# Performance work log

Measured on AMD Instinct MI355X. Metric: run time of the kernel, lower is better.

The kernel has to match this reference:

```python
import jax, jax.numpy as jnp
import numpy as np
from jax import lax

EPS = 1e-6

def rms_norm(x, w):
    return x * lax.rsqrt(jnp.mean(x * x, axis=-1, keepdims=True) + EPS) * w

def rec_layer(x, conv_w, conv_b, Wr_w, Wr_b, Wi_w, Wi_b, log_a, out_w, norm_w):
    # x: [B, L, d]; depthwise causal conv, kernel size 4
    B, L, d = x.shape
    xc = lax.conv_general_dilated(
        x.transpose(0, 2, 1), conv_w, window_strides=(1,), padding=[(3, 0)],
        dimension_numbers=("NCH", "OIH", "NCH"), feature_group_count=d)
    x_conv = xc.transpose(0, 2, 1) + conv_b  # [B, L, d]
    r_t = jax.nn.sigmoid(x_conv @ Wr_w.T + Wr_b)
    i_t = jax.nn.sigmoid(x_conv @ Wi_w.T + Wi_b)
    a_base = jax.nn.sigmoid(log_a)  # [d]
    a_t = jnp.power(a_base, 8.0 * r_t)  # [B, L, d]
    u_t = i_t * x_conv

    def step(h, au):
        a, u = au
        h = a * h + jnp.sqrt(jnp.clip(1.0 - a * a, 0.0, None)) * u
        return h, h

    _, hs = lax.scan(step, jnp.zeros((B, d), x.dtype),
                     (a_t.transpose(1, 0, 2), u_t.transpose(1, 0, 2)))
    out = hs.transpose(1, 0, 2)  # [B, L, d]
    return rms_norm(out @ out_w.T, norm_w)

def setup_inputs() -> dict:
    B, L, M, d, do = 8, 2048, 256, 1024, 256
    key = jax.random.key(0)
    ks = jax.random.split(key, 24)
    inp = {
        "concept_out": jax.random.normal(ks[0], (B, M, d), jnp.float32),
        "encoder_out": jax.random.normal(ks[1], (B, L, d), jnp.float32),
        "boundary_probs": jax.random.uniform(ks[2], (B, L), jnp.float32),
        "boundary_idx": jnp.sort(jax.random.randint(ks[3], (B, M), 0, L, jnp.int32), axis=1),
        "gate_w": jax.random.normal(ks[4], (d, d), jnp.float32) * 0.02,
        "gate_b": jnp.zeros((d,), jnp.float32),
        "down_w": jax.random.normal(ks[5], (do, d), jnp.float32) * 0.02,
        "up_w": jax.random.normal(ks[6], (d, do), jnp.float32) * 0.02,
        "norm_out_w": jnp.ones((d,), jnp.float32),
        "rec_conv_w": jax.random.normal(ks[7], (3, do, 1, 4), jnp.float32) * 0.02,
        "rec_conv_b": jnp.zeros((3, do), jnp.float32),
        "rec_Wr_w": jax.random.normal(ks[8], (3, do, do), jnp.float32) * 0.02,
        "rec_Wr_b": jnp.zeros((3, do), jnp.float32),
        "rec_Wi_w": jax.random.normal(ks[9], (3, do, do), jnp.float32) * 0.02,
        "rec_Wi_b": jnp.zeros((3, do), jnp.float32),
        "rec_log_a": jnp.full((3, do), 7.5, jnp.float32),
        "rec_out_w": jax.random.normal(ks[10], (3, do, do), jnp.float32) * 0.02,
        "rec_norm_w": jnp.ones((3, do), jnp.float32),
    }
    return inp

def reference(concept_out, encoder_out, boundary_probs, boundary_idx,
              gate_w, gate_b, down_w, up_w, norm_out_w,
              rec_conv_w, rec_conv_b, rec_Wr_w, rec_Wr_b,
              rec_Wi_w, rec_Wi_b, rec_log_a, rec_out_w, rec_norm_w):
    B, L, d = encoder_out.shape
    M = concept_out.shape[1]
    # 1. EMA smoothing over boundaries
    p_at_bounds = jnp.take_along_axis(boundary_probs, boundary_idx, axis=1)  # [B, M]

    def ema_step(h, pc):
        p_i, c_i = pc  # [B], [B, d]
        h = p_i[:, None] * c_i + (1.0 - p_i[:, None]) * h
        return h, h

    _, sm = lax.scan(ema_step, jnp.zeros((B, d), concept_out.dtype),
                     (p_at_bounds.T, concept_out.transpose(1, 0, 2)))
    smoothed = sm.transpose(1, 0, 2)  # [B, M, d]
    # 2. Plug-back via searchsorted (== torch.bucketize right=True)
    arange_L = jnp.arange(L)
    counts = jax.vmap(lambda bi: jnp.searchsorted(bi, arange_L, side="right"))(boundary_idx)
    bucket = jnp.clip(counts - 1, 0, None)  # [B, L]
    plugback = jnp.take_along_axis(smoothed, bucket[..., None], axis=1)  # [B, L, d]
    # 3. Gated residual
    gate = jax.nn.sigmoid(encoder_out @ gate_w.T + gate_b)
    h = (1.0 - boundary_probs[..., None]) * gate * encoder_out + plugback
    # 4. Decoder recurrence
    h = h @ down_w.T
    for k in range(3):
        h = rec_layer(h, rec_conv_w[k], rec_conv_b[k], rec_Wr_w[k], rec_Wr_b[k],
                      rec_Wi_w[k], rec_Wi_b[k], rec_log_a[k], rec_out_w[k], rec_norm_w[k])
    h = h @ up_w.T
    return rms_norm(h, norm_out_w)
```

## Files before the change

kernel.cpp:

```cpp
#include <hip/hip_runtime.h>
#include <hip/hip_bf16.h>
#include <stdint.h>

typedef __attribute__((ext_vector_type(8))) short short8;
typedef __attribute__((ext_vector_type(4))) float f32x4;
typedef __hip_bfloat16 bf16;

#define NB   8
#define LSEQ 2048
#define NM   256
#define DMODEL 1024
#define DO   256
#define BLR  16384
#define NCH  64
#define CLK  32

__device__ __forceinline__ float sigm(float x) { return 1.f / (1.f + __expf(-x)); }

__device__ __forceinline__ void gl_lds16(const void* g, void* l) {
  __builtin_amdgcn_global_load_lds((const __attribute__((address_space(1))) void*)g,
                                   (__attribute__((address_space(3))) void*)l, 16, 0, 0);
}

__device__ __forceinline__ short8 ds_read128(const bf16* p) {
  short8 r;
  unsigned a = (unsigned)(uintptr_t)(const __attribute__((address_space(3))) bf16*)p;
  asm volatile("ds_read_b128 %0, %1" : "=v"(r) : "v"(a));
  return r;
}

__device__ __forceinline__ unsigned short bf16bits(float v) {
  bf16 b = __float2bfloat16(v);
  return *(unsigned short*)&b;
}
__device__ __forceinline__ float bits2f(unsigned short u) {
  bf16 b = *(bf16*)&u;
  return __bfloat162float(b);
}


__global__ __launch_bounds__(256) void prep_kernel(
    const float* __restrict__ encoder_out, ushort4* __restrict__ encb4,
    const float* __restrict__ gate_w, const float* __restrict__ down_w,
    const float* __restrict__ up_w, const float* __restrict__ wr_w,
    const float* __restrict__ wi_w, const float* __restrict__ ow_w,
    const float* __restrict__ log_a,
    bf16* __restrict__ gate_wb, bf16* __restrict__ down_wb, bf16* __restrict__ up_wb,
    bf16* __restrict__ wrb, bf16* __restrict__ wib, bf16* __restrict__ owb,
    float* __restrict__ e8) {
  int i = blockIdx.x * 256 + threadIdx.x;
  if (i < 4194304) {
    float4 v = ((const float4*)encoder_out)[i];
    ushort4 o;
    o.x = bf16bits(v.x); o.y = bf16bits(v.y); o.z = bf16bits(v.z); o.w = bf16bits(v.w);
    encb4[i] = o;
    return;
  }
  i -= 4194304;
  if (i < 1048576) { gate_wb[i] = __float2bfloat16(gate_w[i]); return; }
  i -= 1048576;
  if (i < 262144) { down_wb[i] = __float2bfloat16(down_w[i]); return; }
  i -= 262144;
  if (i < 262144) { up_wb[i] = __float2bfloat16(up_w[i]); return; }
  i -= 262144;
  if (i < 196608) { wrb[i] = __float2bfloat16(wr_w[i]); return; }
  i -= 196608;
  if (i < 196608) { wib[i] = __float2bfloat16(wi_w[i]); return; }
  i -= 196608;
  if (i < 196608) { owb[i] = __float2bfloat16(ow_w[i]); return; }
  i -= 196608;
  if (i < 768) {
    float ab = 1.f / (1.f + expf(-log_a[i]));
    e8[i] = 8.f * log2f(ab);
  }
}


__global__ __launch_bounds__(256) void ema_bucket_kernel(const float* __restrict__ cpt,
                                                         const float* __restrict__ bprobs,
                                                         const int* __restrict__ bidx,
                                                         float* __restrict__ smoothed,
                                                         int* __restrict__ bucket) {
  if (blockIdx.x < NB * 4) {
    int b = blockIdx.x >> 2;
    int c = ((blockIdx.x & 3) << 8) + threadIdx.x;
    __shared__ float p[NM];
    p[threadIdx.x] = bprobs[b * LSEQ + bidx[b * NM + threadIdx.x]];
    __syncthreads();
    const float* cp = cpt + (size_t)b * NM * DMODEL + c;
    float* sp = smoothed + (size_t)b * NM * DMODEL + c;
    float h = 0.f;
    for (int m = 0; m < NM; ++m) {
      float pm = p[m];
      h = pm * cp[(size_t)m * DMODEL] + (1.f - pm) * h;
      sp[(size_t)m * DMODEL] = h;
    }
  } else {
    int i = (blockIdx.x - NB * 4) * 256 + threadIdx.x;
    int b = i >> 11, l = i & 2047;
    const int* bi = bidx + b * NM;
    int lo = 0, hi = NM;
    while (lo < hi) {
      int mid = (lo + hi) >> 1;
      if (bi[mid] <= l) lo = mid + 1; else hi = mid;
    }
    int v = lo - 1;
    bucket[i] = v < 0 ? 0 : v;
  }
}


__global__ __launch_bounds__(256) void gate_plug_kernel(bf16* __restrict__ h0,
                                                        const bf16* __restrict__ encb,
                                                        const float* __restrict__ gbias,
                                                        const float* __restrict__ bprobs,
                                                        const int* __restrict__ bucket,
                                                        const float* __restrict__ smoothed) {
  const int m = blockIdx.x;
  const int t = threadIdx.x;
  const int b = m >> 11;
  const float pm1 = 1.f - bprobs[m];
  const float* srow = smoothed + ((size_t)(b * NM + bucket[m])) * DMODEL + t * 4;
  const size_t base = (size_t)m * DMODEL + t * 4;
  ushort4 gr = *(const ushort4*)(h0 + base);
  ushort4 er = *(const ushort4*)(encb + base);
  float4 sm4 = *(const float4*)srow;
  float4 gb4 = *(const float4*)(gbias + t * 4);
  ushort4 o;
  o.x = bf16bits(pm1 * sigm(bits2f(gr.x) + gb4.x) * bits2f(er.x) + sm4.x);
  o.y = bf16bits(pm1 * sigm(bits2f(gr.y) + gb4.y) * bits2f(er.y) + sm4.y);
  o.z = bf16bits(pm1 * sigm(bits2f(gr.z) + gb4.z) * bits2f(er.z) + sm4.z);
  o.w = bf16bits(pm1 * sigm(bits2f(gr.w) + gb4.w) * bits2f(er.w) + sm4.w);
  *(ushort4*)(h0 + base) = o;
}


__global__ __launch_bounds__(256) void conv_kernel(const bf16* __restrict__ x,
                                                   const float* __restrict__ cw,
                                                   const float* __restrict__ cb,
                                                   bf16* __restrict__ xcb) {
  int i4 = blockIdx.x * 256 + threadIdx.x;
  int cg = i4 & 63;
  int bl = i4 >> 6;
  int l = bl & 2047;
  int c0 = cg << 2;
  float wf[4][4];
#pragma unroll
  for (int cc = 0; cc < 4; ++cc) {
    float4 w4 = ((const float4*)cw)[c0 + cc];
    wf[cc][0] = w4.x; wf[cc][1] = w4.y; wf[cc][2] = w4.z; wf[cc][3] = w4.w;
  }
  float4 cb4 = *(const float4*)(cb + c0);
  float s0 = cb4.x, s1 = cb4.y, s2 = cb4.z, s3 = cb4.w;
#pragma unroll
  for (int kk = 0; kk < 4; ++kk) {
    int ll = l - 3 + kk;
    if (ll >= 0) {
      ushort4 xv = *(const ushort4*)(x + (size_t)(bl + kk - 3) * DO + c0);
      s0 += wf[0][kk] * bits2f(xv.x);
      s1 += wf[1][kk] * bits2f(xv.y);
      s2 += wf[2][kk] * bits2f(xv.z);
      s3 += wf[3][kk] * bits2f(xv.w);
    }
  }
  ushort4 o;
  o.x = bf16bits(s0); o.y = bf16bits(s1); o.z = bf16bits(s2); o.w = bf16bits(s3);
  *(ushort4*)(xcb + (size_t)bl * DO + c0) = o;
}


__global__ __launch_bounds__(256) void scan_p1(const unsigned int* __restrict__ ds,
                                               float2* __restrict__ AS) {
  int b = blockIdx.x / NCH, ch = blockIdx.x % NCH, c = threadIdx.x;
  size_t base = ((size_t)b * LSEQ + ch * CLK) * DO + c;
  float A = 1.f, S = 0.f;
  for (int t = 0; t < CLK; ++t) {
    unsigned int u = ds[base + (size_t)t * DO];
    float d = bits2f((unsigned short)(u & 0xffff));
    float s = bits2f((unsigned short)(u >> 16));
    float a = 1.f - d;
    A *= a;
    S = __builtin_fmaf(a, S, s);
  }
  AS[blockIdx.x * DO + c] = make_float2(A, S);
}

__global__ __launch_bounds__(256) void scan_p2(const unsigned int* __restrict__ ds,
                                               const float2* __restrict__ AS,
                                               bf16* __restrict__ hs) {
  int b = blockIdx.x / NCH, ch = blockIdx.x % NCH, c = threadIdx.x;
  float h = 0.f;
  for (int j = 0; j < ch; ++j) {
    float2 as = AS[(b * NCH + j) * DO + c];
    h = __builtin_fmaf(as.x, h, as.y);
  }
  size_t base = ((size_t)b * LSEQ + ch * CLK) * DO + c;
  for (int t = 0; t < CLK; ++t) {
    unsigned int u = ds[base + (size_t)t * DO];
    float d = bits2f((unsigned short)(u & 0xffff));
    float s = bits2f((unsigned short)(u >> 16));
    h = __builtin_fmaf(-d, h, h) + s;
    hs[base + (size_t)t * DO] = __float2bfloat16(h);
  }
}


__global__ __launch_bounds__(256) void rmsnorm1024_kernel(const bf16* __restrict__ in,
                                                          const float* __restrict__ w,
                                                          float* __restrict__ out) {
  int row = blockIdx.x, t = threadIdx.x;
  ushort4 raw = ((const ushort4*)(in + (size_t)row * 1024))[t];
  float v0 = bits2f(raw.x), v1 = bits2f(raw.y), v2 = bits2f(raw.z), v3 = bits2f(raw.w);
  float ss = v0 * v0 + v1 * v1 + v2 * v2 + v3 * v3;
#pragma unroll
  for (int ofs = 32; ofs > 0; ofs >>= 1) ss += __shfl_down(ss, ofs, 64);
  __shared__ float wsum[4];
  if ((t & 63) == 0) wsum[t >> 6] = ss;
  __syncthreads();
  float tot = wsum[0] + wsum[1] + wsum[2] + wsum[3];
  float sc = rsqrtf(tot * (1.f / 1024.f) + 1e-6f);
  float4 wv = ((const float4*)w)[t];
  float4 o;
  o.x = v0 * sc * wv.x; o.y = v1 * sc * wv.y;
  o.z = v2 * sc * wv.z; o.w = v3 * sc * wv.w;
  ((float4*)(out + (size_t)row * 1024))[t] = o;
}


template <int NC, int KC>
__global__ __launch_bounds__(256, 4) void gemm_t64(const bf16* __restrict__ A,
                                                   const bf16* __restrict__ W,
                                                   bf16* __restrict__ outb) {
  __shared__ __align__(16) bf16 As[64 * 64];
  __shared__ __align__(16) bf16 Bs[128 * 64];
  const int t = threadIdx.x;
  const int lane = t & 63;
  const int wv = t >> 6;
  const int wm = wv >> 1, wn = wv & 1;
  const int quad = lane >> 4, l16 = lane & 15;
  const int bm = blockIdx.x << 6, bn = blockIdx.y << 7;

  f32x4 acc[2][4] = {};

  for (int k0 = 0; k0 < KC; k0 += 64) {
    __syncthreads();
#pragma unroll
    for (int i = 0; i < 2; ++i) {
      int slot = i * 256 + t;
      int m = slot >> 3, lk8 = (slot & 7) ^ (m & 7);
      gl_lds16(A + (size_t)(bm + m) * KC + k0 + lk8 * 8, As + slot * 8);
    }
#pragma unroll
    for (int i = 0; i < 4; ++i) {
      int slot = i * 256 + t;
      int n = slot >> 3, lk8 = (slot & 7) ^ (n & 7);
      gl_lds16(W + (size_t)(bn + n) * KC + k0 + lk8 * 8, Bs + slot * 8);
    }
    __syncthreads();
#pragma unroll
    for (int ks = 0; ks < 2; ++ks) {
      short8 af[2], bfr[4];
#pragma unroll
      for (int i = 0; i < 2; ++i) {
        int m = wm * 32 + i * 16 + l16;
        int pa = (ks * 4 + quad) ^ (m & 7);
        af[i] = *(const short8*)(As + m * 64 + pa * 8);
      }
#pragma unroll
      for (int j = 0; j < 4; ++j) {
        int n = wn * 64 + j * 16 + l16;
        int pb = (ks * 4 + quad) ^ (n & 7);
        bfr[j] = *(const short8*)(Bs + n * 64 + pb * 8);
      }
#pragma unroll
      for (int i = 0; i < 2; ++i)
#pragma unroll
        for (int j = 0; j < 4; ++j)
          acc[i][j] = __builtin_amdgcn_mfma_f32_16x16x32_bf16(af[i], bfr[j], acc[i][j], 0, 0, 0);
    }
  }

#pragma unroll
  for (int i = 0; i < 2; ++i)
#pragma unroll
    for (int j = 0; j < 4; ++j)
#pragma unroll
      for (int r = 0; r < 4; ++r) {
        int m = bm + wm * 32 + i * 16 + quad * 4 + r;
        int n = bn + wn * 64 + j * 16 + l16;
        outb[(size_t)m * NC + n] = __float2bfloat16(acc[i][j][r]);
      }
}


template <int KC>
__global__ __launch_bounds__(512, 2) void gemm256(const bf16* __restrict__ Ag,
                                                  const bf16* __restrict__ W,
                                                  bf16* __restrict__ outb) {
  __shared__ __align__(16) bf16 lds[2][4][128 * 64];
  const int t = threadIdx.x;
  const int lane = t & 63;
  const int wv = t >> 6;
  const int wm = wv >> 2, wn = wv & 3;
  const int quad = lane >> 4, l16 = lane & 15;
  const int bm = blockIdx.x << 8, bn = blockIdx.y << 8;
  constexpr int KT = KC >> 6;
  constexpr int KM = KT - 1;

  const int rr = t >> 3;
  const int cc = (t & 7) ^ (rr & 7);

  f32x4 acc[8][4] = {};
  short8 af[4][2], bfr[2][2];

#define STAGE_A(BUF, H, KTI)                                                      \
  {                                                                               \
    int kk = ((KTI) & KM) << 6;                                                   \
    const bf16* s0 = Ag + (size_t)(bm + (H) * 64 + rr) * KC + kk + cc * 8;        \
    gl_lds16(s0, &lds[BUF][H][t * 8]);                                            \
    const bf16* s1 = Ag + (size_t)(bm + (H) * 64 + rr + 128) * KC + kk + cc * 8;  \
    gl_lds16(s1, &lds[BUF][H][(512 + t) * 8]);                                    \
  }
#define STAGE_B(BUF, H, KTI)                                                      \
  {                                                                               \
    int kk = ((KTI) & KM) << 6;                                                   \
    int n0 = (H) * 32 + (rr & 31) + ((rr >> 5) << 6);                             \
    const bf16* s0 = W + (size_t)(bn + n0) * KC + kk + cc * 8;                    \
    gl_lds16(s0, &lds[BUF][2 + (H)][t * 8]);                                      \
    const bf16* s1 = W + (size_t)(bn + n0 + 128) * KC + kk + cc * 8;              \
    gl_lds16(s1, &lds[BUF][2 + (H)][(512 + t) * 8]);                              \
  }
#define LD_A(BUF, MG)                                                             \
  _Pragma("unroll") for (int ii = 0; ii < 4; ++ii) {                              \
    int r = wm * 64 + ii * 16 + l16;                                              \
    _Pragma("unroll") for (int ks = 0; ks < 2; ++ks) {                            \
      int ch = (ks * 4 + quad) ^ (r & 7);                                         \
      af[ii][ks] = ds_read128(&lds[BUF][MG][(r * 8 + ch) * 8]);                   \
    }                                                                             \
  }
#define LD_B(BUF, NG)                                                             \
  _Pragma("unroll") for (int jj = 0; jj < 2; ++jj) {                              \
    int r = wn * 32 + jj * 16 + l16;                                              \
    _Pragma("unroll") for (int ks = 0; ks < 2; ++ks) {                            \
      int ch = (ks * 4 + quad) ^ (r & 7);                                         \
      bfr[jj][ks] = ds_read128(&lds[BUF][2 + (NG)][(r * 8 + ch) * 8]);            \
    }                                                                             \
  }
#define MMA(MG, NG)                                                               \
  _Pragma("unroll") for (int ks = 0; ks < 2; ++ks)                                \
  _Pragma("unroll") for (int ii = 0; ii < 4; ++ii)                                \
  _Pragma("unroll") for (int jj = 0; jj < 2; ++jj)                                \
    acc[(MG) * 4 + ii][(NG) * 2 + jj] = __builtin_amdgcn_mfma_f32_16x16x32_bf16(  \
        af[ii][ks], bfr[jj][ks], acc[(MG) * 4 + ii][(NG) * 2 + jj], 0, 0, 0);
#define BARR __builtin_amdgcn_s_barrier()
#define WAIT_LGKM asm volatile("s_waitcnt lgkmcnt(0)" ::: "memory")
#define WAIT_VM6 asm volatile("s_waitcnt vmcnt(6)" ::: "memory")
#define SBAR __builtin_amdgcn_sched_barrier(0)
#define PH(MG, NG)                   \
  BARR; WAIT_LGKM; SBAR;             \
  __builtin_amdgcn_s_setprio(1);     \
  MMA(MG, NG);                       \
  __builtin_amdgcn_s_setprio(0);     \
  SBAR;                              \
  BARR;
#define PH_V(MG, NG)                 \
  BARR; WAIT_LGKM; SBAR;             \
  __builtin_amdgcn_s_setprio(1);     \
  MMA(MG, NG);                       \
  __builtin_amdgcn_s_setprio(0);     \
  SBAR;                              \
  WAIT_VM6;                          \
  BARR;

  STAGE_A(0, 0, 0) STAGE_A(0, 1, 0) STAGE_B(0, 0, 0) STAGE_B(0, 1, 0)
  STAGE_A(1, 0, 1) STAGE_A(1, 1, 1) STAGE_B(1, 1, 1)
  WAIT_VM6;
  BARR;

#pragma unroll 1
  for (int it = 0; it < (KT >> 1); ++it) {
    const int kt = it * 2;
    LD_A(0, 0) LD_B(0, 0)
    STAGE_B(1, 0, kt + 1)
    PH(0, 0)
    LD_B(0, 1)
    STAGE_A(0, 0, kt + 2)
    PH(0, 1)
    LD_A(0, 1)
    STAGE_B(0, 1, kt + 2)
    PH(1, 1)
    LD_B(0, 0)
    STAGE_A(0, 1, kt + 2)
    PH_V(1, 0)
    LD_A(1, 0) LD_B(1, 0)
    STAGE_B(0, 0, kt + 2)
    PH(0, 0)
    LD_B(1, 1)
    STAGE_A(1, 0, kt + 3)
    PH(0, 1)
    LD_A(1, 1)
    STAGE_B(1, 1, kt + 3)
    PH(1, 1)
    LD_B(1, 0)
    STAGE_A(1, 1, kt + 3)
    PH_V(1, 0)
  }

#undef STAGE_A
#undef STAGE_B
#undef LD_A
#undef LD_B
#undef MMA
#undef BARR
#undef WAIT_LGKM
#undef WAIT_VM6
#undef SBAR
#undef PH
#undef PH_V

#pragma unroll
  for (int i = 0; i < 8; ++i) {
#pragma unroll
    for (int j = 0; j < 4; ++j) {
#pragma unroll
      for (int r = 0; r < 4; ++r) {
        int m = bm + wm * 128 + i * 16 + quad * 4 + r;
        int n = bn + wn * 64 + j * 16 + l16;
        outb[(size_t)m * DMODEL + n] = __float2bfloat16(acc[i][j][r]);
      }
    }
  }
}


__global__ __launch_bounds__(256, 4) void gemm_ri(const bf16* __restrict__ A,
                                                  const bf16* __restrict__ Wr,
                                                  const bf16* __restrict__ Wi,
                                                  const float* __restrict__ rbias,
                                                  const float* __restrict__ ibias,
                                                  const float* __restrict__ e8,
                                                  unsigned int* __restrict__ ds_out) {
  __shared__ __align__(16) bf16 As[32 * 64];
  __shared__ __align__(16) bf16 Br[128 * 64];
  __shared__ __align__(16) bf16 Bi[128 * 64];
  const int t = threadIdx.x;
  const int lane = t & 63;
  const int wv = t >> 6;
  const int wm = wv >> 1, wn = wv & 1;
  const int quad = lane >> 4, l16 = lane & 15;
  const int bm = blockIdx.x << 5;
  const int bn = blockIdx.y << 7;

  f32x4 ar[4] = {};
  f32x4 ai[4] = {};

  for (int k0 = 0; k0 < DO; k0 += 64) {
    __syncthreads();
    {
      int m = t >> 3, lk8 = (t & 7) ^ (m & 7);
      gl_lds16(A + (size_t)(bm + m) * DO + k0 + lk8 * 8, As + t * 8);
    }
#pragma unroll
    for (int i = 0; i < 4; ++i) {
      int slot = i * 256 + t;
      int n = slot >> 3, lk8 = (slot & 7) ^ (n & 7);
      gl_lds16(Wr + (size_t)(bn + n) * DO + k0 + lk8 * 8, Br + slot * 8);
      gl_lds16(Wi + (size_t)(bn + n) * DO + k0 + lk8 * 8, Bi + slot * 8);
    }
    __syncthreads();
#pragma unroll
    for (int ks = 0; ks < 2; ++ks) {
      int m = wm * 16 + l16;
      int pa = (ks * 4 + quad) ^ (m & 7);
      short8 af = *(const short8*)(As + m * 64 + pa * 8);
#pragma unroll
      for (int j = 0; j < 4; ++j) {
        int n = wn * 64 + j * 16 + l16;
        int pb = (ks * 4 + quad) ^ (n & 7);
        short8 br = *(const short8*)(Br + n * 64 + pb * 8);
        short8 bi = *(const short8*)(Bi + n * 64 + pb * 8);
        ar[j] = __builtin_amdgcn_mfma_f32_16x16x32_bf16(af, br, ar[j], 0, 0, 0);
        ai[j] = __builtin_amdgcn_mfma_f32_16x16x32_bf16(af, bi, ai[j], 0, 0, 0);
      }
    }
  }

#pragma unroll
  for (int j = 0; j < 4; ++j) {
    int n = bn + wn * 64 + j * 16 + l16;
    float rb = rbias[n], ib = ibias[n], e8n = e8[n];
#pragma unroll
    for (int r = 0; r < 4; ++r) {
      int m = bm + wm * 16 + quad * 4 + r;
      size_t idx = (size_t)m * DO + n;
      float rv = sigm(ar[j][r] + rb);
      float a = exp2f(rv * e8n);
      float d = 1.f - a;
      float iv = sigm(ai[j][r] + ib);
      float xc = __bfloat162float(A[idx]);
      float s = sqrtf(fmaxf(1.f - a * a, 0.f)) * iv * xc;
      ds_out[idx] = (unsigned int)bf16bits(d) | ((unsigned int)bf16bits(s) << 16);
    }
  }
}


__global__ __launch_bounds__(256, 4) void gemm_on(const bf16* __restrict__ A,
                                                  const bf16* __restrict__ W,
                                                  const float* __restrict__ rnw,
                                                  bf16* __restrict__ xb) {
  __shared__ __align__(16) bf16 As[32 * 64];
  __shared__ __align__(16) bf16 Bs[256 * 64];
  __shared__ float red[4][32];
  const int t = threadIdx.x;
  const int lane = t & 63;
  const int wn = t >> 6;
  const int quad = lane >> 4, l16 = lane & 15;
  const int bm = blockIdx.x << 5;

  f32x4 acc[2][4] = {};

  for (int k0 = 0; k0 < DO; k0 += 64) {
    __syncthreads();
    {
      int m = t >> 3, lk8 = (t & 7) ^ (m & 7);
      gl_lds16(A + (size_t)(bm + m) * DO + k0 + lk8 * 8, As + t * 8);
    }
#pragma unroll
    for (int i = 0; i < 8; ++i) {
      int slot = i * 256 + t;
      int n = slot >> 3, lk8 = (slot & 7) ^ (n & 7);
      gl_lds16(W + (size_t)n * DO + k0 + lk8 * 8, Bs + slot * 8);
    }
    __syncthreads();
#pragma unroll
    for (int ks = 0; ks < 2; ++ks) {
      short8 af[2], bfr[4];
#pragma unroll
      for (int i = 0; i < 2; ++i) {
        int m = i * 16 + l16;
        int pa = (ks * 4 + quad) ^ (m & 7);
        af[i] = *(const short8*)(As + m * 64 + pa * 8);
      }
#pragma unroll
      for (int j = 0; j < 4; ++j) {
        int n = wn * 64 + j * 16 + l16;
        int pb = (ks * 4 + quad) ^ (n & 7);
        bfr[j] = *(const short8*)(Bs + n * 64 + pb * 8);
      }
#pragma unroll
      for (int i = 0; i < 2; ++i)
#pragma unroll
        for (int j = 0; j < 4; ++j)
          acc[i][j] = __builtin_amdgcn_mfma_f32_16x16x32_bf16(af[i], bfr[j], acc[i][j], 0, 0, 0);
    }
  }

  float part[2][4];
#pragma unroll
  for (int i = 0; i < 2; ++i)
#pragma unroll
    for (int r = 0; r < 4; ++r) {
      float s = 0.f;
#pragma unroll
      for (int j = 0; j < 4; ++j) s += acc[i][j][r] * acc[i][j][r];
      part[i][r] = s;
    }
#pragma unroll
  for (int mask = 1; mask <= 8; mask <<= 1)
#pragma unroll
    for (int i = 0; i < 2; ++i)
#pragma unroll
      for (int r = 0; r < 4; ++r) part[i][r] += __shfl_xor(part[i][r], mask, 64);
  if (l16 == 0) {
#pragma unroll
    for (int i = 0; i < 2; ++i)
#pragma unroll
      for (int r = 0; r < 4; ++r) red[wn][i * 16 + quad * 4 + r] = part[i][r];
  }
  __syncthreads();
#pragma unroll
  for (int i = 0; i < 2; ++i) {
#pragma unroll
    for (int r = 0; r < 4; ++r) {
      int ml = i * 16 + quad * 4 + r;
      float tot = red[0][ml] + red[1][ml] + red[2][ml] + red[3][ml];
      float sc = rsqrtf(tot * (1.f / 256.f) + 1e-6f);
#pragma unroll
      for (int j = 0; j < 4; ++j) {
        int n = wn * 64 + j * 16 + l16;
        xb[(size_t)(bm + ml) * DO + n] = __float2bfloat16(acc[i][j][r] * sc * rnw[n]);
      }
    }
  }
}


extern "C" void kernel_launch(void* const* d_in, const int* in_sizes, int n_in,
                              void* d_out, int out_size, void* d_ws, size_t ws_size,
                              hipStream_t stream) {
  const float* concept_out = (const float*)d_in[0];
  const float* encoder_out = (const float*)d_in[1];
  const float* bprobs      = (const float*)d_in[2];
  const int*   bidx        = (const int*)d_in[3];
  const float* gate_w      = (const float*)d_in[4];
  const float* gate_b      = (const float*)d_in[5];
  const float* down_w      = (const float*)d_in[6];
  const float* up_w        = (const float*)d_in[7];
  const float* norm_out_w  = (const float*)d_in[8];
  const float* rc_w        = (const float*)d_in[9];
  const float* rc_b        = (const float*)d_in[10];
  const float* wr_w        = (const float*)d_in[11];
  const float* wr_b        = (const float*)d_in[12];
  const float* wi_w        = (const float*)d_in[13];
  const float* wi_b        = (const float*)d_in[14];
  const float* log_a       = (const float*)d_in[15];
  const float* ow_w        = (const float*)d_in[16];
  const float* rn_w        = (const float*)d_in[17];
  float* out = (float*)d_out;
  (void)in_sizes; (void)n_in; (void)out_size; (void)ws_size;

  char* base = (char*)d_ws;
  size_t off = 0;
  auto alloc = [&](size_t bytes) -> char* {
    char* p = base + off;
    off += (bytes + 255) & ~(size_t)255;
    return p;
  };
  float* smoothed = (float*)alloc((size_t)NB * NM * DMODEL * 4);
  int*   bucket   = (int*)alloc((size_t)BLR * 4);
  bf16*  gate_wb  = (bf16*)alloc((size_t)DMODEL * DMODEL * 2);
  bf16*  down_wb  = (bf16*)alloc((size_t)DO * DMODEL * 2);
  bf16*  up_wb    = (bf16*)alloc((size_t)DMODEL * DO * 2);
  bf16*  wrb      = (bf16*)alloc((size_t)3 * DO * DO * 2);
  bf16*  wib      = (bf16*)alloc((size_t)3 * DO * DO * 2);
  bf16*  owb      = (bf16*)alloc((size_t)3 * DO * DO * 2);
  float* e8       = (float*)alloc(3 * DO * 4);
  float2* ASsum   = (float2*)alloc((size_t)NB * NCH * DO * 8);
  bf16*  xb       = (bf16*)alloc((size_t)BLR * DO * 2);

  const size_t SZ_ENC   = (size_t)BLR * DMODEL * 2;
  const size_t SZ_XCONV = (size_t)BLR * DO * 2;
  const size_t SZ_DS    = (size_t)BLR * DO * 4;
  char* RA = alloc(2 * SZ_ENC);
  bf16*  encb = (bf16*)RA;
  bf16*  h0b  = (bf16*)(RA + SZ_ENC);
  bf16*         xconvb = (bf16*)RA;
  unsigned int* dsbuf  = (unsigned int*)(RA + SZ_XCONV);
  bf16*         hsb    = (bf16*)(RA + SZ_XCONV + SZ_DS);
  bf16*  tmp2b  = (bf16*)RA;

  prep_kernel<<<(4194304 + 2163456 + 255) / 256, 256, 0, stream>>>(
      encoder_out, (ushort4*)encb,
      gate_w, down_w, up_w, wr_w, wi_w, ow_w, log_a,
      gate_wb, down_wb, up_wb, wrb, wib, owb, e8);
  ema_bucket_kernel<<<NB * 4 + BLR / 256, 256, 0, stream>>>(
      concept_out, bprobs, bidx, smoothed, bucket);

  gemm256<DMODEL><<<dim3(BLR / 256, DMODEL / 256), 512, 0, stream>>>(encb, gate_wb, h0b);
  gate_plug_kernel<<<BLR, 256, 0, stream>>>(h0b, encb, gate_b, bprobs, bucket, smoothed);

  gemm_t64<DO, DMODEL><<<dim3(BLR / 64, DO / 128), 256, 0, stream>>>(h0b, down_wb, xb);

  for (int k = 0; k < 3; ++k) {
    conv_kernel<<<BLR * 64 / 256, 256, 0, stream>>>(xb, rc_w + k * DO * 4, rc_b + k * DO, xconvb);
    gemm_ri<<<dim3(BLR / 32, DO / 128), 256, 0, stream>>>(
        xconvb, wrb + k * DO * DO, wib + k * DO * DO,
        wr_b + k * DO, wi_b + k * DO, e8 + k * DO, dsbuf);
    scan_p1<<<NB * NCH, 256, 0, stream>>>(dsbuf, ASsum);
    scan_p2<<<NB * NCH, 256, 0, stream>>>(dsbuf, ASsum, hsb);
    gemm_on<<<BLR / 32, 256, 0, stream>>>(hsb, owb + k * DO * DO, rn_w + k * DO, xb);
  }

  gemm_t64<DMODEL, DO><<<dim3(BLR / 64, DMODEL / 128), 256, 0, stream>>>(xb, up_wb, tmp2b);
  rmsnorm1024_kernel<<<BLR, 256, 0, stream>>>(tmp2b, norm_out_w, out);
}
```

Baseline: 476.8 us.

## Parallelize EMA smoothing with chunked two-pass scan and retune scan chunking

```diff
diff --git a/kernel.cpp b/kernel.cpp
--- a/kernel.cpp
+++ b/kernel.cpp
@@ -12,8 +12,10 @@
 #define DMODEL 1024
 #define DO   256
 #define BLR  16384
-#define NCH  64
-#define CLK  32
+#define NCH  32
+#define CLK  64
+#define EMC  8
+#define EMCL 32
 
 __device__ __forceinline__ float sigm(float x) { return 1.f / (1.f + __expf(-x)); }
 
@@ -76,27 +78,31 @@
 }
 
 
-__global__ __launch_bounds__(256) void ema_bucket_kernel(const float* __restrict__ cpt,
-                                                         const float* __restrict__ bprobs,
-                                                         const int* __restrict__ bidx,
-                                                         float* __restrict__ smoothed,
-                                                         int* __restrict__ bucket) {
-  if (blockIdx.x < NB * 4) {
-    int b = blockIdx.x >> 2;
-    int c = ((blockIdx.x & 3) << 8) + threadIdx.x;
-    __shared__ float p[NM];
-    p[threadIdx.x] = bprobs[b * LSEQ + bidx[b * NM + threadIdx.x]];
+__global__ __launch_bounds__(256) void ema_p1(const float* __restrict__ cpt,
+                                              const float* __restrict__ bprobs,
+                                              const int* __restrict__ bidx,
+                                              float2* __restrict__ ASe,
+                                              int* __restrict__ bucket) {
+  if (blockIdx.x < 256) {
+    int blk = blockIdx.x;
+    int b = blk >> 5, cq = (blk >> 3) & 3, ch = blk & 7;
+    int c = cq * 256 + threadIdx.x;
+    __shared__ float pl[EMCL];
+    if (threadIdx.x < EMCL) {
+      int m = ch * EMCL + threadIdx.x;
+      pl[threadIdx.x] = bprobs[b * LSEQ + bidx[b * NM + m]];
+    }
     __syncthreads();
-    const float* cp = cpt + (size_t)b * NM * DMODEL + c;
-    float* sp = smoothed + (size_t)b * NM * DMODEL + c;
-    float h = 0.f;
-    for (int m = 0; m < NM; ++m) {
-      float pm = p[m];
-      h = pm * cp[(size_t)m * DMODEL] + (1.f - pm) * h;
-      sp[(size_t)m * DMODEL] = h;
-    }
+    const float* cp = cpt + ((size_t)b * NM + ch * EMCL) * DMODEL + c;
+    float A = 1.f, S = 0.f;
+    for (int mm = 0; mm < EMCL; ++mm) {
+      float pm = pl[mm];
+      A *= (1.f - pm);
+      S = pm * cp[(size_t)mm * DMODEL] + (1.f - pm) * S;
+    }
+    ASe[((size_t)(b * EMC + ch)) * DMODEL + c] = make_float2(A, S);
   } else {
-    int i = (blockIdx.x - NB * 4) * 256 + threadIdx.x;
+    int i = (blockIdx.x - 256) * 256 + threadIdx.x;
     int b = i >> 11, l = i & 2047;
     const int* bi = bidx + b * NM;
     int lo = 0, hi = NM;
@@ -106,6 +112,34 @@
     }
     int v = lo - 1;
     bucket[i] = v < 0 ? 0 : v;
+  }
+}
+
+__global__ __launch_bounds__(256) void ema_p2(const float* __restrict__ cpt,
+                                              const float* __restrict__ bprobs,
+                                              const int* __restrict__ bidx,
+                                              const float2* __restrict__ ASe,
+                                              float* __restrict__ smoothed) {
+  int blk = blockIdx.x;
+  int b = blk >> 5, cq = (blk >> 3) & 3, ch = blk & 7;
+  int c = cq * 256 + threadIdx.x;
+  __shared__ float pl[EMCL];
+  if (threadIdx.x < EMCL) {
+    int m = ch * EMCL + threadIdx.x;
+    pl[threadIdx.x] = bprobs[b * LSEQ + bidx[b * NM + m]];
+  }
+  __syncthreads();
+  float h = 0.f;
+  for (int j = 0; j < ch; ++j) {
+    float2 as = ASe[((size_t)(b * EMC + j)) * DMODEL + c];
+    h = __builtin_fmaf(as.x, h, as.y);
+  }
+  const float* cp = cpt + ((size_t)b * NM + ch * EMCL) * DMODEL + c;
+  float* sp = smoothed + ((size_t)b * NM + ch * EMCL) * DMODEL + c;
+  for (int mm = 0; mm < EMCL; ++mm) {
+    float pm = pl[mm];
+    h = pm * cp[(size_t)mm * DMODEL] + (1.f - pm) * h;
+    sp[(size_t)mm * DMODEL] = h;
   }
 }
 
@@ -637,6 +671,7 @@
   bf16*  owb      = (bf16*)alloc((size_t)3 * DO * DO * 2);
   float* e8       = (float*)alloc(3 * DO * 4);
   float2* ASsum   = (float2*)alloc((size_t)NB * NCH * DO * 8);
+  float2* ASe     = (float2*)alloc((size_t)NB * EMC * DMODEL * 8);
   bf16*  xb       = (bf16*)alloc((size_t)BLR * DO * 2);
 
   const size_t SZ_ENC   = (size_t)BLR * DMODEL * 2;
@@ -654,8 +689,8 @@
       encoder_out, (ushort4*)encb,
       gate_w, down_w, up_w, wr_w, wi_w, ow_w, log_a,
       gate_wb, down_wb, up_wb, wrb, wib, owb, e8);
-  ema_bucket_kernel<<<NB * 4 + BLR / 256, 256, 0, stream>>>(
-      concept_out, bprobs, bidx, smoothed, bucket);
+  ema_p1<<<256 + BLR / 256, 256, 0, stream>>>(concept_out, bprobs, bidx, ASe, bucket);
+  ema_p2<<<256, 256, 0, stream>>>(concept_out, bprobs, bidx, ASe, smoothed);
 
   gemm256<DMODEL><<<dim3(BLR / 256, DMODEL / 256), 512, 0, stream>>>(encb, gate_wb, h0b);
   gate_plug_kernel<<<BLR, 256, 0, stream>>>(h0b, encb, gate_b, bprobs, bucket, smoothed);
```

New measurement: 458.1 us. -3.9%, faster.
